# Kernel optimization log

Hardware: AMD Instinct MI355X
Metric: run time of the kernel (lower is better)

Reference implementation:

```python
import jax, jax.numpy as jnp
import numpy as np

H = 512

def setup_inputs() -> dict:
    key = jax.random.key(0)
    k1, k2, k3, k4 = jax.random.split(key, 4)
    B, S_dec, S_enc = 8, 2048, 2048
    encoder_output = jax.random.normal(k1, (B, S_enc, H), dtype=jnp.float32)
    decoder_output = jax.random.normal(k2, (B, S_dec, H), dtype=jnp.float32)
    # nn.Bilinear(H, H, 1): weight [1, H, H], bias [1]; init U(-1/sqrt(H), 1/sqrt(H))
    bound = 1.0 / np.sqrt(H)
    W = jax.random.uniform(k3, (1, H, H), dtype=jnp.float32, minval=-bound, maxval=bound)
    b = jax.random.uniform(k4, (1,), dtype=jnp.float32, minval=-bound, maxval=bound)
    return {"encoder_output": encoder_output, "decoder_output": decoder_output, "W": W, "b": b}

def reference(encoder_output, decoder_output, W, b):
    # Original: scores[b,d,e] = Bilinear(enc[b,e], dec[b,d]) = enc[b,e] @ W[0] @ dec[b,d] + bias
    # Computed as two GEMMs instead of expanding to [B, S_dec, S_enc, H].
    encW = jnp.einsum('beh,hg->beg', encoder_output, W[0])   # [B, S_enc, H]
    scores = jnp.einsum('beg,bdg->bde', encW, decoder_output) + b[0]  # [B, S_dec, S_enc]
    return scores
```

## Files before the change

### kernel.cpp

```cpp
#include <hip/hip_runtime.h>

typedef __attribute__((ext_vector_type(8))) short short8;
typedef __attribute__((ext_vector_type(4))) float f32x4;
typedef __attribute__((ext_vector_type(8))) unsigned short ushort8;

__device__ __forceinline__ unsigned short f2bf(float x) {
  union { float f; unsigned u; } v; v.f = x;
  unsigned r = v.u + 0x7fffu + ((v.u >> 16) & 1u);
  return (unsigned short)(r >> 16);
}

__global__ __launch_bounds__(256) void wt_kernel(
    const float* __restrict__ W, unsigned short* __restrict__ Wt) {
  __shared__ float s[64][65];
  int g0 = blockIdx.x * 64, h0 = blockIdx.y * 64;
  int tx = threadIdx.x & 63, ty = threadIdx.x >> 6;
#pragma unroll
  for (int rr = 0; rr < 16; ++rr) {
    int h = ty * 16 + rr;
    s[h][tx] = W[(long)(h0 + h) * 512 + g0 + tx];
  }
  __syncthreads();
#pragma unroll
  for (int rr = 0; rr < 16; ++rr) {
    int g = ty * 16 + rr;
    Wt[(long)(g0 + g) * 512 + h0 + tx] = f2bf(s[tx][g]);
  }
}

__global__ __launch_bounds__(256) void gemm1_plus_cvtdec(
    const float* __restrict__ enc, const unsigned short* __restrict__ Wt,
    unsigned short* __restrict__ encW,
    const float* __restrict__ dec, unsigned short* __restrict__ dec_bf) {
  if (blockIdx.x >= 512) {
    int i = (blockIdx.x - 512) * 256 + threadIdx.x;
    const float4* p = (const float4*)(dec + (long)i * 8);
    float4 a = p[0], b = p[1];
    ushort8 o;
    o[0] = f2bf(a.x); o[1] = f2bf(a.y); o[2] = f2bf(a.z); o[3] = f2bf(a.w);
    o[4] = f2bf(b.x); o[5] = f2bf(b.y); o[6] = f2bf(b.z); o[7] = f2bf(b.w);
    *(ushort8*)(dec_bf + (long)i * 8) = o;
    return;
  }

  constexpr int K = 512, N = 512, BK = 32;
  __shared__ __align__(16) short As[128 * BK];
  __shared__ __align__(16) short Bs[128 * BK];

  const int g = blockIdx.x;
  const int work = (g & 7) * 64 + (g >> 3);
  const int bxm = work >> 2, byn = work & 3;

  const int tid = threadIdx.x;
  const int wave = tid >> 6, lane = tid & 63;
  const int wm = wave >> 1, wn = wave & 1;
  const int r = lane & 15, q = lane >> 4;

  const float* Ab = enc + (long)bxm * 128 * K;
  const unsigned short* Bb = Wt + (long)byn * 128 * K;

  const int srow = tid >> 1, shalf = tid & 1;
  const float* arow = Ab + (long)srow * K + shalf * 16;

  f32x4 acc[4][4] = {};
  float4 av[4];
#pragma unroll
  for (int j = 0; j < 4; ++j) av[j] = ((const float4*)arow)[j];

  for (int kt = 0; kt < K; kt += BK) {
    ushort8 o0, o1;
    o0[0] = f2bf(av[0].x); o0[1] = f2bf(av[0].y); o0[2] = f2bf(av[0].z); o0[3] = f2bf(av[0].w);
    o0[4] = f2bf(av[1].x); o0[5] = f2bf(av[1].y); o0[6] = f2bf(av[1].z); o0[7] = f2bf(av[1].w);
    o1[0] = f2bf(av[2].x); o1[1] = f2bf(av[2].y); o1[2] = f2bf(av[2].z); o1[3] = f2bf(av[2].w);
    o1[4] = f2bf(av[3].x); o1[5] = f2bf(av[3].y); o1[6] = f2bf(av[3].z); o1[7] = f2bf(av[3].w);
    *(ushort8*)&As[srow * BK + shalf * 16 + 0] = o0;
    *(ushort8*)&As[srow * BK + shalf * 16 + 8] = o1;

#pragma unroll
    for (int j = 0; j < 2; ++j) {
      int c = (j * 4 + wave) * 64 + lane;
      int row = c >> 2;
      int coff = (c & 3) * 8;
      __builtin_amdgcn_global_load_lds(
          (const __attribute__((address_space(1))) void*)(Bb + (long)row * K + kt + coff),
          (__attribute__((address_space(3))) void*)(Bs + (j * 4 + wave) * 512),
          16, 0, 0);
    }
    __syncthreads();

    short8 af[4], bfr[4];
#pragma unroll
    for (int m = 0; m < 4; ++m)
      af[m] = *(const short8*)&As[(wm * 64 + m * 16 + r) * BK + q * 8];
#pragma unroll
    for (int n = 0; n < 4; ++n)
      bfr[n] = *(const short8*)&Bs[(wn * 64 + n * 16 + r) * BK + q * 8];

    if (kt + BK < K) {
      const float* ap = arow + kt + BK;
#pragma unroll
      for (int j = 0; j < 4; ++j) av[j] = ((const float4*)ap)[j];
    }

#pragma unroll
    for (int m = 0; m < 4; ++m)
#pragma unroll
      for (int n = 0; n < 4; ++n)
        acc[m][n] = __builtin_amdgcn_mfma_f32_16x16x32_bf16(af[m], bfr[n], acc[m][n], 0, 0, 0);
    __syncthreads();
  }

  const long rowbase = (long)bxm * 128 + wm * 64;
  const long colbase = (long)byn * 128 + wn * 64;
#pragma unroll
  for (int m = 0; m < 4; ++m)
#pragma unroll
    for (int n = 0; n < 4; ++n)
#pragma unroll
      for (int j = 0; j < 4; ++j) {
        long row = rowbase + m * 16 + q * 4 + j;
        long col = colbase + n * 16 + r;
        encW[row * (long)N + col] = f2bf(acc[m][n][j]);
      }
}

__global__ __launch_bounds__(256, 4) void gemm2_m97(
    const unsigned short* __restrict__ A,
    const unsigned short* __restrict__ Bt,
    float* __restrict__ C, const float* __restrict__ bias) {
  constexpr int K = 512, BK = 32;
  __shared__ __align__(16) short As[128 * BK];
  __shared__ __align__(16) short Bs[128 * BK];

  int flat = blockIdx.x;
  int sw = (flat & 7) * 256 + (flat >> 3);
  int z = sw >> 8, bx = (sw >> 4) & 15, by = sw & 15;

  const int tid = threadIdx.x;
  const int wave = tid >> 6, lane = tid & 63;
  const int wm = wave >> 1, wn = wave & 1;
  const int r = lane & 15, q = lane >> 4;

  const unsigned short* Ab = A + ((long)z * 2048 + bx * 128) * 512;
  const unsigned short* Bb = Bt + ((long)z * 2048 + by * 128) * 512;

  f32x4 acc[4][4] = {};

  for (int kt = 0; kt < K; kt += BK) {
#pragma unroll
    for (int j = 0; j < 2; ++j) {
      int c = (j * 4 + wave) * 64 + lane;
      int row = c >> 2;
      int coff = (c & 3) * 8;
      __builtin_amdgcn_global_load_lds(
          (const __attribute__((address_space(1))) void*)(Ab + (long)row * K + kt + coff),
          (__attribute__((address_space(3))) void*)(As + (j * 4 + wave) * 512),
          16, 0, 0);
      __builtin_amdgcn_global_load_lds(
          (const __attribute__((address_space(1))) void*)(Bb + (long)row * K + kt + coff),
          (__attribute__((address_space(3))) void*)(Bs + (j * 4 + wave) * 512),
          16, 0, 0);
    }
    __syncthreads();

    short8 af[4], bfr[4];
#pragma unroll
    for (int m = 0; m < 4; ++m)
      af[m] = *(const short8*)&As[(wm * 64 + m * 16 + r) * BK + q * 8];
#pragma unroll
    for (int n = 0; n < 4; ++n)
      bfr[n] = *(const short8*)&Bs[(wn * 64 + n * 16 + r) * BK + q * 8];

#pragma unroll
    for (int m = 0; m < 4; ++m)
#pragma unroll
      for (int n = 0; n < 4; ++n)
        acc[m][n] = __builtin_amdgcn_mfma_f32_16x16x32_bf16(af[m], bfr[n], acc[m][n], 0, 0, 0);
    __syncthreads();
  }

  const float bv = bias[0];
  float* Cb = C + ((long)z * 2048 + bx * 128 + wm * 64) * 2048 + by * 128 + wn * 64;
#pragma unroll
  for (int m = 0; m < 4; ++m)
#pragma unroll
    for (int n = 0; n < 4; ++n)
#pragma unroll
      for (int j = 0; j < 4; ++j)
        Cb[(long)(m * 16 + q * 4 + j) * 2048 + n * 16 + r] = acc[m][n][j] + bv;
}

extern "C" void kernel_launch(void* const* d_in, const int* in_sizes, int n_in,
                              void* d_out, int out_size, void* d_ws, size_t ws_size,
                              hipStream_t stream) {
  const float* enc  = (const float*)d_in[0];
  const float* dec  = (const float*)d_in[1];
  const float* W    = (const float*)d_in[2];
  const float* bias = (const float*)d_in[3];
  float* out = (float*)d_out;

  constexpr int Bn = 8, S = 2048, H = 512;
  constexpr long NE = (long)Bn * S * H;

  unsigned short* dec_bf = (unsigned short*)d_ws;
  unsigned short* Wt     = dec_bf + NE;
  unsigned short* encW   = Wt + (long)H * H;

  wt_kernel<<<dim3(8, 8), 256, 0, stream>>>(W, Wt);

  gemm1_plus_cvtdec<<<dim3(512 + 4096, 1, 1), 256, 0, stream>>>(
      enc, Wt, encW, dec, dec_bf);

  gemm2_m97<<<dim3(2048, 1, 1), 256, 0, stream>>>(dec_bf, encW, out, bias);
}
```

Baseline: 83.25 us.

## Widen gemm2 tile to 128x256 with XOR-swizzled LDS layout

The second GEMM now uses 128x256 output tiles, so each wave computes 64x128 with 32 MFMA accumulators, and the grid drops to 1024 blocks. LDS staging is reorganised into 16-row chunks with an XOR swizzle on the column offset to reduce bank conflicts on fragment reads. Block-to-batch mapping changes so consecutive blocks share the same output tile position across batches. More accumulator registers lower occupancy (launch bounds 2), and the larger tile cuts the grid's parallelism.

```diff
diff --git a/kernel.cpp b/kernel.cpp
--- a/kernel.cpp
+++ b/kernel.cpp
@@ -124,70 +124,78 @@
       }
 }
 
-__global__ __launch_bounds__(256, 4) void gemm2_m97(
+__global__ __launch_bounds__(256, 2) void gemm2_w256(
     const unsigned short* __restrict__ A,
     const unsigned short* __restrict__ Bt,
     float* __restrict__ C, const float* __restrict__ bias) {
-  constexpr int K = 512, BK = 32;
-  __shared__ __align__(16) short As[128 * BK];
-  __shared__ __align__(16) short Bs[128 * BK];
-
-  int flat = blockIdx.x;
-  int sw = (flat & 7) * 256 + (flat >> 3);
-  int z = sw >> 8, bx = (sw >> 4) & 15, by = sw & 15;
+  constexpr int K = 512;
+  __shared__ __align__(16) char As[8192];
+  __shared__ __align__(16) char Bs[16384];
+
+  const int flat = blockIdx.x;
+  const int z = flat & 7;
+  const int work = flat >> 3;
+  const int by = work & 7, bx = work >> 3;
 
   const int tid = threadIdx.x;
   const int wave = tid >> 6, lane = tid & 63;
   const int wm = wave >> 1, wn = wave & 1;
-  const int r = lane & 15, q = lane >> 4;
+  const int base_r = lane & 15, q = lane >> 4;
+  const int lconst = base_r * 64 + ((q * 16) ^ ((base_r & 8) << 2));
+  const int srow = lane >> 2;
+  const int scol = ((lane & 3) * 8) ^ (((lane >> 5) & 1) << 4);
 
   const unsigned short* Ab = A + ((long)z * 2048 + bx * 128) * 512;
-  const unsigned short* Bb = Bt + ((long)z * 2048 + by * 128) * 512;
-
-  f32x4 acc[4][4] = {};
-
-  for (int kt = 0; kt < K; kt += BK) {
-#pragma unroll
-    for (int j = 0; j < 2; ++j) {
-      int c = (j * 4 + wave) * 64 + lane;
-      int row = c >> 2;
-      int coff = (c & 3) * 8;
-      __builtin_amdgcn_global_load_lds(
-          (const __attribute__((address_space(1))) void*)(Ab + (long)row * K + kt + coff),
-          (__attribute__((address_space(3))) void*)(As + (j * 4 + wave) * 512),
-          16, 0, 0);
-      __builtin_amdgcn_global_load_lds(
-          (const __attribute__((address_space(1))) void*)(Bb + (long)row * K + kt + coff),
-          (__attribute__((address_space(3))) void*)(Bs + (j * 4 + wave) * 512),
-          16, 0, 0);
+  const unsigned short* Bb = Bt + ((long)z * 2048 + by * 256) * 512;
+
+  f32x4 acc[4][8] = {};
+
+  for (int kt = 0; kt < K; kt += 32) {
+#pragma unroll
+    for (int j = 0; j < 6; ++j) {
+      int c = wave * 6 + j;
+      if (c < 8) {
+        __builtin_amdgcn_global_load_lds(
+            (const __attribute__((address_space(1))) void*)(
+                Ab + (long)(c * 16 + srow) * 512 + kt + scol),
+            (__attribute__((address_space(3))) void*)(As + (c << 10)),
+            16, 0, 0);
+      } else {
+        int cb = c - 8;
+        __builtin_amdgcn_global_load_lds(
+            (const __attribute__((address_space(1))) void*)(
+                Bb + (long)(cb * 16 + srow) * 512 + kt + scol),
+            (__attribute__((address_space(3))) void*)(Bs + (cb << 10)),
+            16, 0, 0);
+      }
     }
     __syncthreads();
 
-    short8 af[4], bfr[4];
-#pragma unroll
-    for (int m = 0; m < 4; ++m)
-      af[m] = *(const short8*)&As[(wm * 64 + m * 16 + r) * BK + q * 8];
-#pragma unroll
-    for (int n = 0; n < 4; ++n)
-      bfr[n] = *(const short8*)&Bs[(wn * 64 + n * 16 + r) * BK + q * 8];
-
-#pragma unroll
-    for (int m = 0; m < 4; ++m)
-#pragma unroll
-      for (int n = 0; n < 4; ++n)
+    short8 af[4], bfr[8];
+#pragma unroll
+    for (int m = 0; m < 4; ++m)
+      af[m] = *(const short8*)(As + ((wm * 4 + m) << 10) + lconst);
+#pragma unroll
+    for (int n = 0; n < 8; ++n)
+      bfr[n] = *(const short8*)(Bs + ((wn * 8 + n) << 10) + lconst);
+
+#pragma unroll
+    for (int m = 0; m < 4; ++m)
+#pragma unroll
+      for (int n = 0; n < 8; ++n)
         acc[m][n] = __builtin_amdgcn_mfma_f32_16x16x32_bf16(af[m], bfr[n], acc[m][n], 0, 0, 0);
     __syncthreads();
   }
 
   const float bv = bias[0];
-  float* Cb = C + ((long)z * 2048 + bx * 128 + wm * 64) * 2048 + by * 128 + wn * 64;
+  float* Cb = C + ((long)z * 2048 + bx * 128 + wm * 64) * 2048 + by * 256 + wn * 128;
 #pragma unroll
   for (int m = 0; m < 4; ++m)
 #pragma unroll
-    for (int n = 0; n < 4; ++n)
+    for (int n = 0; n < 8; ++n)
 #pragma unroll
       for (int j = 0; j < 4; ++j)
-        Cb[(long)(m * 16 + q * 4 + j) * 2048 + n * 16 + r] = acc[m][n][j] + bv;
+        Cb[(long)(m * 16 + q * 4 + j) * 2048 + n * 16 + base_r] = acc[m][n][j] + bv;
 }
 
 extern "C" void kernel_launch(void* const* d_in, const int* in_sizes, int n_in,
@@ -211,5 +219,5 @@
   gemm1_plus_cvtdec<<<dim3(512 + 4096, 1, 1), 256, 0, stream>>>(
       enc, Wt, encW, dec, dec_bf);
 
-  gemm2_m97<<<dim3(2048, 1, 1), 256, 0, stream>>>(dec_bf, encW, out, bias);
-}
+  gemm2_w256<<<dim3(1024, 1, 1), 256, 0, stream>>>(dec_bf, encW, out, bias);
+}
```

Result: no change. 84.73 us (+1.8%).
